# Optimization experiments

Hardware: AMD Instinct MI355X
Metric: run time of the kernel (lower is better)

Reference implementation:

```python
import jax, jax.numpy as jnp
import numpy as np

EPS = 1e-8

def _normalize(a):
    return a / jnp.clip(jnp.linalg.norm(a, axis=-1, keepdims=True), EPS)

def _cosine(a, b):
    # pairwise cosine similarity: [Na, d] x [Nb, d] -> [Na, Nb]
    return _normalize(a) @ _normalize(b).T

def setup_inputs() -> dict:
    key = jax.random.key(0)
    n, k, q, d = 100, 5, 75, 4096
    x = jax.random.normal(key, (n * (k + q), d), dtype=jnp.float32)
    tao = jnp.full((1,), 10.0, dtype=jnp.float32)
    return {"x": x, "tao": tao, "n": n, "k": k, "q": q}

def reference(x, tao, n, k, q):
    d = x.shape[-1]
    x = x.reshape(n, k + q, d)
    support = x[:, :k]                      # [n, k, d]
    query = x[:, k:].reshape(n * q, d)      # [NQ, d]
    NQ = n * q
    proto = support.mean(axis=1)            # [n, d]

    pre_sim = _cosine(query, proto)         # [NQ, n]
    pre_label = jnp.argmax(pre_sim, axis=1) # [NQ]

    # vectorized per-class masked softmax aggregation (replaces Python loop)
    cls_ids = jnp.arange(n)
    mask = pre_label[None, :] == cls_ids[:, None]            # [n, NQ]
    logits_q = jnp.where(mask, pre_sim.T, -jnp.inf)          # [n, NQ]
    proto_n = _normalize(proto)
    self_sim = jnp.sum(proto_n * proto_n, axis=-1)           # [n], cosine(proto, proto)
    logits = jnp.concatenate([logits_q, self_sim[:, None]], axis=1)  # [n, NQ+1]
    w = jax.nn.softmax(logits, axis=1)                       # [n, NQ+1]
    adapted_proto = w[:, :NQ] @ query + w[:, NQ:] * proto    # [n, d]

    sim = _cosine(query, adapted_proto)                      # [NQ, n]
    return tao.reshape(()) * sim
```

## Files before the change

### kernel.cpp

```cpp
#include <hip/hip_runtime.h>
#include <hip/hip_bf16.h>
#include <math.h>

#define NQUERY 7500
#define NCLS   100
#define DIM    4096
#define KQ     75
#define KSUP   5
#define RPC    80
#define MPAD   7552
#define NPAD   112
#define CAPQ   256
#define RCAP   2048
#define EPSF   1e-8f
#define SELEM  845824
#define SLICE_BYTES 3383296u

typedef __attribute__((ext_vector_type(8))) short bf16x8;
typedef __attribute__((ext_vector_type(4))) short s16x4;
typedef __attribute__((ext_vector_type(4))) float f32x4;

__device__ __forceinline__ int xrow_of_query(int j) {
    return (j / KQ) * RPC + KSUP + (j % KQ);
}
__device__ __forceinline__ short bf16t(float x) {
    union { float f; unsigned u; } v; v.f = x;
    return (short)(v.u >> 16);
}
__device__ __forceinline__ float bf16hi(float x) {
    union { float f; unsigned u; } v; v.f = x;
    v.u &= 0xFFFF0000u; return v.f;
}
__device__ __forceinline__ void gload_lds16(const short* g, short* l) {
    __builtin_amdgcn_global_load_lds(
        (const __attribute__((address_space(1))) unsigned int*)g,
        (__attribute__((address_space(3))) unsigned int*)l, 16, 0, 0);
}

__device__ __forceinline__ size_t tile_off(int nt, int lm, int i) {
    return (((size_t)(nt * 128 + (i >> 5)) * 4 + ((i >> 3) & 3)) * 16 + lm) * 8 + (i & 7);
}

__global__ __launch_bounds__(256) void k_proto(const float* __restrict__ x,
        float* __restrict__ proto, short* __restrict__ Phi, short* __restrict__ Plo,
        float* __restrict__ es) {
    const int c = blockIdx.x, t = threadIdx.x;
    const int nt = c >> 4, lm = c & 15;
    if (c >= NCLS) {
        for (int g = t; g < 512; g += 256) {
            const int kstep = g >> 2, kq = g & 3;
            size_t o = (((size_t)(nt * 128 + kstep) * 4 + kq) * 16 + lm) * 8;
            bf16x8 z = {0,0,0,0,0,0,0,0};
            *(bf16x8*)(Phi + o) = z;
            *(bf16x8*)(Plo + o) = z;
        }
        if (t == 0) es[c] = 0.f;
        return;
    }
    __shared__ float red[4];
    __shared__ float s_inv;
    const float* b0 = x + (size_t)(c * RPC) * DIM;
    float v[16];
    float ssq = 0.f;
#pragma unroll
    for (int p = 0; p < 4; ++p) {
        const int i = p * 1024 + t * 4;
        f32x4 s = {0.f, 0.f, 0.f, 0.f};
#pragma unroll
        for (int r = 0; r < KSUP; ++r)
            s += *(const f32x4*)(b0 + (size_t)r * DIM + i);
        s = s / 5.0f;
        *(f32x4*)&v[p*4] = s;
        *(f32x4*)(proto + (size_t)c*DIM + i) = s;
        ssq += s[0]*s[0] + s[1]*s[1] + s[2]*s[2] + s[3]*s[3];
    }
    for (int o = 32; o; o >>= 1) ssq += __shfl_down(ssq, o);
    if ((t & 63) == 0) red[t >> 6] = ssq;
    __syncthreads();
    if (t == 0) {
        float tot = red[0] + red[1] + red[2] + red[3];
        float inv = 1.f / fmaxf(sqrtf(tot), EPSF);
        s_inv = inv;
        es[c] = expf(tot * inv * inv);
    }
    __syncthreads();
    const float inv = s_inv;
#pragma unroll
    for (int p = 0; p < 4; ++p) {
        const int i = p * 1024 + t * 4;
        s16x4 h, l;
#pragma unroll
        for (int e = 0; e < 4; ++e) {
            float pn = v[p*4+e] * inv;
            float hh = bf16hi(pn);
            h[e] = bf16t(pn);
            l[e] = bf16t(pn - hh);
        }
        const size_t o = tile_off(nt, lm, i);
        *(s16x4*)(Phi + o) = h;
        *(s16x4*)(Plo + o) = l;
    }
}

template<int TNKS>
__global__ __launch_bounds__(256) void k_gemm1(const float* __restrict__ x,
        const short* __restrict__ Phi, const short* __restrict__ Plo,
        float* __restrict__ Spart, float* __restrict__ nq2) {
    constexpr int KST = 128 / TNKS;
    constexpr int NG  = KST / 2;
    __shared__ short bbuf[28 * 512];
    const int bx = blockIdx.x, kz = blockIdx.y;
    const int w = threadIdx.x >> 6, lane = threadIdx.x & 63;
    const int lm = lane & 15, kq = lane >> 4;
    const int mt = bx * 4 + w;
    const int j = mt * 16 + lm;
    const int jc = j < NQUERY ? j : NQUERY - 1;
    const float* pa = x + (size_t)xrow_of_query(jc) * DIM + kq * 8;
    const int ks0 = kz * KST;

    f32x4 acc[7];
#pragma unroll
    for (int nt = 0; nt < 7; ++nt) acc[nt] = (f32x4){0.f,0.f,0.f,0.f};
    float ssq = 0.f;

    for (int g = 0; g < NG; ++g) {
        const int gk = ks0 + g * 2;
#pragma unroll
        for (int p = 0; p < 7; ++p) {
            const int cid = w * 7 + p;
            const int s = cid / 14, r = cid % 14, nt = r >> 1, hl = r & 1;
            const short* gsrc = (hl ? Plo : Phi) + ((size_t)(nt * 128 + gk + s) << 9);
            gload_lds16(gsrc + lane * 8, &bbuf[(cid << 9) + lane * 8]);
        }
        __syncthreads();
#pragma unroll
        for (int s = 0; s < 2; ++s) {
            const float* pas = pa + (gk + s) * 32;
            f32x4 f0 = *(const f32x4*)(pas);
            f32x4 f1 = *(const f32x4*)(pas + 4);
            float fv[8] = {f0[0],f0[1],f0[2],f0[3],f1[0],f1[1],f1[2],f1[3]};
            bf16x8 ah, al;
#pragma unroll
            for (int e = 0; e < 8; ++e) {
                float xx = fv[e];
                ssq += xx * xx;
                float hh = bf16hi(xx);
                ah[e] = bf16t(xx);
                al[e] = bf16t(xx - hh);
            }
#pragma unroll
            for (int nt = 0; nt < 7; ++nt) {
                const bf16x8 bh = *(const bf16x8*)(&bbuf[((s*14 + nt*2 + 0) << 9) + lane * 8]);
                const bf16x8 bl = *(const bf16x8*)(&bbuf[((s*14 + nt*2 + 1) << 9) + lane * 8]);
                acc[nt] = __builtin_amdgcn_mfma_f32_16x16x32_bf16(ah, bh, acc[nt], 0, 0, 0);
                acc[nt] = __builtin_amdgcn_mfma_f32_16x16x32_bf16(ah, bl, acc[nt], 0, 0, 0);
                acc[nt] = __builtin_amdgcn_mfma_f32_16x16x32_bf16(al, bh, acc[nt], 0, 0, 0);
            }
        }
        __syncthreads();
    }
    float s2 = ssq;
    s2 += __shfl_xor(s2, 16);
    s2 += __shfl_xor(s2, 32);
    if (kq == 0 && j < NQUERY) atomicAdd(&nq2[j], s2);

    float* sp = Spart + (size_t)kz * SELEM + (size_t)(mt * 16) * NPAD;
#pragma unroll
    for (int nt = 0; nt < 7; ++nt)
#pragma unroll
        for (int r = 0; r < 4; ++r)
            sp[(size_t)(kq * 4 + r) * NPAD + nt * 16 + lm] = acc[nt][r];
}

__global__ __launch_bounds__(256) void k_reduce1(const float* __restrict__ Spart,
        float* __restrict__ Sred, int nks) {
    const int idx = blockIdx.x * 256 + threadIdx.x;
    const size_t e = (size_t)idx * 4;
    f32x4 s = {0.f, 0.f, 0.f, 0.f};
    for (int kz = 0; kz < nks; ++kz)
        s += *(const f32x4*)(Spart + (size_t)kz * SELEM + e);
    *(f32x4*)(Sred + e) = s;
}

__global__ __launch_bounds__(256) void k_argmax(const float* __restrict__ S,
        const float* __restrict__ nq2, int* __restrict__ label, float* __restrict__ coef,
        float* __restrict__ invq, int* __restrict__ rcnt, int* __restrict__ rlist) {
    const int j = blockIdx.x * 256 + threadIdx.x;
    if (j >= NQUERY) return;
    const float* row = S + (size_t)j * NPAD;
    float m1 = -1e30f, m2 = -1e30f;
    int i1 = 0, i2 = 0;
    for (int c = 0; c < NCLS; ++c) {
        float v = row[c];
        if (v > m1) { m2 = m1; i2 = i1; m1 = v; i1 = c; }
        else if (v > m2) { m2 = v; i2 = c; }
    }
    const float inv = 1.f / fmaxf(sqrtf(nq2[j]), EPSF);
    invq[j] = inv;
    label[j] = i1;
    coef[j] = expf(m1 * inv);
    if ((m1 - m2) * inv < 1e-4f) {
        int p = atomicAdd(rcnt, 1);
        if (p < RCAP) rlist[p] = j | (i1 << 13) | (i2 << 20);
    }
}

__global__ __launch_bounds__(64) void k_refine(const float* __restrict__ x,
        const float* __restrict__ S, const float* __restrict__ invq,
        int* __restrict__ label, float* __restrict__ coef,
        const int* __restrict__ rcnt, const int* __restrict__ rlist) {
    const int cnt = min(*rcnt, RCAP);
    const int lane = threadIdx.x;
    for (int e = blockIdx.x; e < cnt; e += gridDim.x) {
        const int pk = rlist[e];
        const int j = pk & 8191, c1 = (pk >> 13) & 127, c2 = (pk >> 20) & 127;
        const float* xq = x + (size_t)xrow_of_query(j) * DIM;
        const int cc[2] = {c1, c2};
        double cosv[2];
#pragma unroll
        for (int s = 0; s < 2; ++s) {
            const float* xb = x + (size_t)(cc[s] * RPC) * DIM;
            double dt = 0.0, pp = 0.0, q2 = 0.0;
            for (int i = lane; i < DIM; i += 64) {
                double p = (double)xb[i] + (double)xb[i + DIM] + (double)xb[i + 2*DIM]
                         + (double)xb[i + 3*DIM] + (double)xb[i + 4*DIM];
                double qv = (double)xq[i];
                dt += p * qv; pp += p * p; q2 += qv * qv;
            }
            for (int o = 32; o; o >>= 1) {
                dt += __shfl_down(dt, o);
                pp += __shfl_down(pp, o);
                q2 += __shfl_down(q2, o);
            }
            cosv[s] = dt / (sqrt(pp) * sqrt(q2));
        }
        if (lane == 0) {
            int win = (cosv[1] > cosv[0] || (cosv[1] == cosv[0] && c2 < c1)) ? c2 : c1;
            if (win != c1) {
                label[j] = win;
                coef[j] = expf(S[(size_t)j * NPAD + win] * invq[j]);
            }
        }
    }
}

__global__ __launch_bounds__(256) void k_lists(const int* __restrict__ label,
        int* __restrict__ cls_cnt, int* __restrict__ cls_list) {
    const int j = blockIdx.x * 256 + threadIdx.x;
    if (j >= NQUERY) return;
    const int c = label[j];
    const int p = atomicAdd(&cls_cnt[c], 1);
    if (p < CAPQ) cls_list[c * CAPQ + p] = j;
}

__global__ __launch_bounds__(128) void k_adapt(const float* __restrict__ x,
        const float* __restrict__ coef, const int* __restrict__ cls_cnt,
        const int* __restrict__ cls_list, float* __restrict__ APpart) {
    const int cx = blockIdx.x, c = blockIdx.y, sl = blockIdx.z;
    const int i0 = cx * 512 + threadIdx.x * 4;
    const int n = min(cls_cnt[c], CAPQ);
    f32x4 acc = {0.f, 0.f, 0.f, 0.f};
    for (int e = sl; e < n; e += 4) {
        const int j = cls_list[c * CAPQ + e];
        const float cf = coef[j];
        const f32x4 v = *(const f32x4*)(x + (size_t)xrow_of_query(j) * DIM + i0);
        acc += v * cf;
    }
    *(f32x4*)(APpart + (size_t)sl * NCLS * DIM + (size_t)c * DIM + i0) = acc;
}

__global__ __launch_bounds__(256) void k_apnorm(const float* __restrict__ APpart,
        const float* __restrict__ proto, const float* __restrict__ es,
        short* __restrict__ APhi) {
    const int c = blockIdx.x, t = threadIdx.x;
    const int nt = c >> 4, lm = c & 15;
    if (c >= NCLS) {
        for (int g = t; g < 512; g += 256) {
            const int kstep = g >> 2, kq = g & 3;
            size_t o = (((size_t)(nt * 128 + kstep) * 4 + kq) * 16 + lm) * 8;
            bf16x8 z = {0,0,0,0,0,0,0,0};
            *(bf16x8*)(APhi + o) = z;
        }
        return;
    }
    __shared__ float red[4];
    __shared__ float s_inv;
    const float e0 = es[c];
    float v[16];
    float ssq = 0.f;
#pragma unroll
    for (int p = 0; p < 4; ++p) {
        const int i = p * 1024 + t * 4;
        f32x4 s = {0.f, 0.f, 0.f, 0.f};
#pragma unroll
        for (int sl = 0; sl < 4; ++sl)
            s += *(const f32x4*)(APpart + (size_t)sl * NCLS * DIM + (size_t)c * DIM + i);
        f32x4 pr = *(const f32x4*)(proto + (size_t)c*DIM + i);
        s += pr * e0;
        *(f32x4*)&v[p*4] = s;
        ssq += s[0]*s[0] + s[1]*s[1] + s[2]*s[2] + s[3]*s[3];
    }
    for (int o = 32; o; o >>= 1) ssq += __shfl_down(ssq, o);
    if ((t & 63) == 0) red[t >> 6] = ssq;
    __syncthreads();
    if (t == 0) {
        float tot = red[0] + red[1] + red[2] + red[3];
        s_inv = 1.f / fmaxf(sqrtf(tot), EPSF);
    }
    __syncthreads();
    const float inv = s_inv;
#pragma unroll
    for (int p = 0; p < 4; ++p) {
        const int i = p * 1024 + t * 4;
        s16x4 h;
#pragma unroll
        for (int e = 0; e < 4; ++e) h[e] = bf16t(v[p*4+e] * inv);
        *(s16x4*)(APhi + tile_off(nt, lm, i)) = h;
    }
}

template<int TNKS>
__global__ __launch_bounds__(256) void k_gemm2(const float* __restrict__ x,
        const short* __restrict__ APhi, float* __restrict__ Opart) {
    constexpr int KST = 128 / TNKS;
    constexpr int NG  = KST / 2;
    __shared__ short bbuf[14 * 512];
    const int bx = blockIdx.x, kz = blockIdx.y;
    const int w = threadIdx.x >> 6, lane = threadIdx.x & 63;
    const int lm = lane & 15, kq = lane >> 4;
    const int mt = bx * 4 + w;
    const int j = mt * 16 + lm;
    const int jc = j < NQUERY ? j : NQUERY - 1;
    const float* pa = x + (size_t)xrow_of_query(jc) * DIM + kq * 8;
    const int ks0 = kz * KST;

    f32x4 acc[7];
#pragma unroll
    for (int nt = 0; nt < 7; ++nt) acc[nt] = (f32x4){0.f,0.f,0.f,0.f};

    for (int g = 0; g < NG; ++g) {
        const int gk = ks0 + g * 2;
#pragma unroll
        for (int p = 0; p < 4; ++p) {
            const int cid = w * 4 + p;
            if (cid < 14) {
                const int s = cid / 7, nt = cid % 7;
                const short* gsrc = APhi + ((size_t)(nt * 128 + gk + s) << 9);
                gload_lds16(gsrc + lane * 8, &bbuf[(cid << 9) + lane * 8]);
            }
        }
        __syncthreads();
#pragma unroll
        for (int s = 0; s < 2; ++s) {
            const float* pas = pa + (gk + s) * 32;
            f32x4 f0 = *(const f32x4*)(pas);
            f32x4 f1 = *(const f32x4*)(pas + 4);
            float fv[8] = {f0[0],f0[1],f0[2],f0[3],f1[0],f1[1],f1[2],f1[3]};
            bf16x8 ah;
#pragma unroll
            for (int e = 0; e < 8; ++e) ah[e] = bf16t(fv[e]);
#pragma unroll
            for (int nt = 0; nt < 7; ++nt) {
                const bf16x8 bh = *(const bf16x8*)(&bbuf[((s*7 + nt) << 9) + lane * 8]);
                acc[nt] = __builtin_amdgcn_mfma_f32_16x16x32_bf16(ah, bh, acc[nt], 0, 0, 0);
            }
        }
        __syncthreads();
    }
    float* op = Opart + (size_t)kz * SELEM + (size_t)(mt * 16) * NPAD;
#pragma unroll
    for (int nt = 0; nt < 7; ++nt)
#pragma unroll
        for (int r = 0; r < 4; ++r)
            op[(size_t)(kq * 4 + r) * NPAD + nt * 16 + lm] = acc[nt][r];
}

__global__ __launch_bounds__(256) void k_reduce2(const float* __restrict__ Opart,
        const float* __restrict__ invq, const float* __restrict__ tao,
        float* __restrict__ out, int nks) {
    const int idx = blockIdx.x * 256 + threadIdx.x;
    if (idx >= NQUERY * 25) return;
    const int j = idx / 25, c4 = (idx % 25) * 4;
    const size_t e = (size_t)j * NPAD + c4;
    f32x4 s = {0.f, 0.f, 0.f, 0.f};
    for (int kz = 0; kz < nks; ++kz)
        s += *(const f32x4*)(Opart + (size_t)kz * SELEM + e);
    const float sc = tao[0] * invq[j];
    *(f32x4*)(out + (size_t)j * NCLS + c4) = s * sc;
}

#define OFF_RCNT   0u
#define OFF_CCNT   256u
#define OFF_NQ2    1792u
#define ZERO_BYTES 32768u
#define OFF_ES     32768u
#define OFF_INVQ   33280u
#define OFF_LABEL  63488u
#define OFF_COEF   93696u
#define OFF_RLIST  123904u
#define OFF_CLIST  132096u
#define OFF_PROTO  234496u
#define OFF_PHI    1872896u
#define OFF_PLO    2790400u
#define OFF_APHI   3707904u
#define OFF_SRED   4625408u
#define OFF_APPART 8008704u
#define OFF_PART   14562304u

extern "C" void kernel_launch(void* const* d_in, const int* in_sizes, int n_in,
                              void* d_out, int out_size, void* d_ws, size_t ws_size,
                              hipStream_t stream) {
    const float* x   = (const float*)d_in[0];
    const float* tao = (const float*)d_in[1];
    char* ws = (char*)d_ws;

    int*   rcnt    = (int*)  (ws + OFF_RCNT);
    int*   ccnt    = (int*)  (ws + OFF_CCNT);
    float* nq2     = (float*)(ws + OFF_NQ2);
    float* es      = (float*)(ws + OFF_ES);
    float* invq    = (float*)(ws + OFF_INVQ);
    int*   label   = (int*)  (ws + OFF_LABEL);
    float* coef    = (float*)(ws + OFF_COEF);
    int*   rlist   = (int*)  (ws + OFF_RLIST);
    int*   clist   = (int*)  (ws + OFF_CLIST);
    float* proto   = (float*)(ws + OFF_PROTO);
    short* Phi     = (short*)(ws + OFF_PHI);
    short* Plo     = (short*)(ws + OFF_PLO);
    short* APhi    = (short*)(ws + OFF_APHI);
    float* Sred    = (float*)(ws + OFF_SRED);
    float* APpart  = (float*)(ws + OFF_APPART);
    float* Part    = (float*)(ws + OFF_PART);

    int nks = 1;
    if (ws_size > (size_t)OFF_PART + SLICE_BYTES) {
        size_t avail = (ws_size - OFF_PART) / SLICE_BYTES;
        nks = avail >= 16 ? 16 : (int)avail;
        while (nks & (nks - 1)) nks &= nks - 1;
    }

    hipMemsetAsync(ws, 0, ZERO_BYTES, stream);

    k_proto <<<NPAD, 256, 0, stream>>>(x, proto, Phi, Plo, es);
    switch (nks) {
        case 16: k_gemm1<16><<<dim3(118, 16), 256, 0, stream>>>(x, Phi, Plo, Part, nq2); break;
        case 8:  k_gemm1<8> <<<dim3(118, 8),  256, 0, stream>>>(x, Phi, Plo, Part, nq2); break;
        case 4:  k_gemm1<4> <<<dim3(118, 4),  256, 0, stream>>>(x, Phi, Plo, Part, nq2); break;
        case 2:  k_gemm1<2> <<<dim3(118, 2),  256, 0, stream>>>(x, Phi, Plo, Part, nq2); break;
        default: k_gemm1<1> <<<dim3(118, 1),  256, 0, stream>>>(x, Phi, Plo, Part, nq2); break;
    }
    k_reduce1<<<826, 256, 0, stream>>>(Part, Sred, nks);
    k_argmax <<<30, 256, 0, stream>>>(Sred, nq2, label, coef, invq, rcnt, rlist);
    k_refine <<<512, 64, 0, stream>>>(x, Sred, invq, label, coef, rcnt, rlist);
    k_lists  <<<30, 256, 0, stream>>>(label, ccnt, clist);
    k_adapt  <<<dim3(8, NCLS, 4), 128, 0, stream>>>(x, coef, ccnt, clist, APpart);
    k_apnorm <<<NPAD, 256, 0, stream>>>(APpart, proto, es, APhi);
    switch (nks) {
        case 16: k_gemm2<16><<<dim3(118, 16), 256, 0, stream>>>(x, APhi, Part); break;
        case 8:  k_gemm2<8> <<<dim3(118, 8),  256, 0, stream>>>(x, APhi, Part); break;
        case 4:  k_gemm2<4> <<<dim3(118, 4),  256, 0, stream>>>(x, APhi, Part); break;
        case 2:  k_gemm2<2> <<<dim3(118, 2),  256, 0, stream>>>(x, APhi, Part); break;
        default: k_gemm2<1> <<<dim3(118, 1),  256, 0, stream>>>(x, APhi, Part); break;
    }
    k_reduce2<<<733, 256, 0, stream>>>(Part, invq, tao, (float*)d_out, nks);
}
```

Measured before the change: 365.1 us.

## Drop split-bf16 first GEMM, unify double-buffered GEMM, fold class lists into argmax

The first similarity GEMM moves from a three-MFMA hi/lo bf16 split to a single bf16 MFMA, so the Plo buffer and its staging go away. Both GEMMs now share one templated kernel that double-buffers the B tile in LDS and prefetches the next A fragment. The per-class list build moves into k_argmax, and k_refine patches the lists for relabelled near-tie queries, which removes the separate k_lists launch. The near-tie threshold is widened to offset the lower argmax precision, at the risk of mislabelling queries or adding more refine work.

```diff
diff --git a/kernel.cpp b/kernel.cpp
--- a/kernel.cpp
+++ b/kernel.cpp
@@ -27,10 +27,6 @@
     union { float f; unsigned u; } v; v.f = x;
     return (short)(v.u >> 16);
 }
-__device__ __forceinline__ float bf16hi(float x) {
-    union { float f; unsigned u; } v; v.f = x;
-    v.u &= 0xFFFF0000u; return v.f;
-}
 __device__ __forceinline__ void gload_lds16(const short* g, short* l) {
     __builtin_amdgcn_global_load_lds(
         (const __attribute__((address_space(1))) unsigned int*)g,
@@ -41,9 +37,20 @@
     return (((size_t)(nt * 128 + (i >> 5)) * 4 + ((i >> 3) & 3)) * 16 + lm) * 8 + (i & 7);
 }
 
+__device__ __forceinline__ void stageB(const short* __restrict__ Bt, int kstep,
+        short* buf, int w, int lane) {
+#pragma unroll
+    for (int p = 0; p < 2; ++p) {
+        const int cid = w * 2 + p;
+        if (cid < 7) {
+            const short* gsrc = Bt + ((size_t)(cid * 128 + kstep) << 9);
+            gload_lds16(gsrc + lane * 8, buf + (cid << 9));
+        }
+    }
+}
+
 __global__ __launch_bounds__(256) void k_proto(const float* __restrict__ x,
-        float* __restrict__ proto, short* __restrict__ Phi, short* __restrict__ Plo,
-        float* __restrict__ es) {
+        float* __restrict__ proto, short* __restrict__ Phi, float* __restrict__ es) {
     const int c = blockIdx.x, t = threadIdx.x;
     const int nt = c >> 4, lm = c & 15;
     if (c >= NCLS) {
@@ -52,7 +59,6 @@
             size_t o = (((size_t)(nt * 128 + kstep) * 4 + kq) * 16 + lm) * 8;
             bf16x8 z = {0,0,0,0,0,0,0,0};
             *(bf16x8*)(Phi + o) = z;
-            *(bf16x8*)(Plo + o) = z;
         }
         if (t == 0) es[c] = 0.f;
         return;
@@ -88,27 +94,18 @@
 #pragma unroll
     for (int p = 0; p < 4; ++p) {
         const int i = p * 1024 + t * 4;
-        s16x4 h, l;
-#pragma unroll
-        for (int e = 0; e < 4; ++e) {
-            float pn = v[p*4+e] * inv;
-            float hh = bf16hi(pn);
-            h[e] = bf16t(pn);
-            l[e] = bf16t(pn - hh);
-        }
-        const size_t o = tile_off(nt, lm, i);
-        *(s16x4*)(Phi + o) = h;
-        *(s16x4*)(Plo + o) = l;
-    }
-}
-
-template<int TNKS>
-__global__ __launch_bounds__(256) void k_gemm1(const float* __restrict__ x,
-        const short* __restrict__ Phi, const short* __restrict__ Plo,
-        float* __restrict__ Spart, float* __restrict__ nq2) {
+        s16x4 h;
+#pragma unroll
+        for (int e = 0; e < 4; ++e) h[e] = bf16t(v[p*4+e] * inv);
+        *(s16x4*)(Phi + tile_off(nt, lm, i)) = h;
+    }
+}
+
+template<int TNKS, bool SSQ>
+__global__ __launch_bounds__(256) void k_gemm(const float* __restrict__ x,
+        const short* __restrict__ Bt, float* __restrict__ Part, float* __restrict__ nq2) {
     constexpr int KST = 128 / TNKS;
-    constexpr int NG  = KST / 2;
-    __shared__ short bbuf[28 * 512];
+    __shared__ short bbuf[2][7 * 512];
     const int bx = blockIdx.x, kz = blockIdx.y;
     const int w = threadIdx.x >> 6, lane = threadIdx.x & 63;
     const int lm = lane & 15, kq = lane >> 4;
@@ -123,48 +120,43 @@
     for (int nt = 0; nt < 7; ++nt) acc[nt] = (f32x4){0.f,0.f,0.f,0.f};
     float ssq = 0.f;
 
-    for (int g = 0; g < NG; ++g) {
-        const int gk = ks0 + g * 2;
-#pragma unroll
-        for (int p = 0; p < 7; ++p) {
-            const int cid = w * 7 + p;
-            const int s = cid / 14, r = cid % 14, nt = r >> 1, hl = r & 1;
-            const short* gsrc = (hl ? Plo : Phi) + ((size_t)(nt * 128 + gk + s) << 9);
-            gload_lds16(gsrc + lane * 8, &bbuf[(cid << 9) + lane * 8]);
+    stageB(Bt, ks0, bbuf[0], w, lane);
+    f32x4 a0 = *(const f32x4*)(pa + ks0 * 32);
+    f32x4 a1 = *(const f32x4*)(pa + ks0 * 32 + 4);
+    __syncthreads();
+
+#pragma unroll
+    for (int s = 0; s < KST; ++s) {
+        const int cur = s & 1;
+        f32x4 n0 = a0, n1 = a1;
+        if (s + 1 < KST) {
+            stageB(Bt, ks0 + s + 1, bbuf[cur ^ 1], w, lane);
+            n0 = *(const f32x4*)(pa + (ks0 + s + 1) * 32);
+            n1 = *(const f32x4*)(pa + (ks0 + s + 1) * 32 + 4);
+        }
+        float fv[8] = {a0[0],a0[1],a0[2],a0[3],a1[0],a1[1],a1[2],a1[3]};
+        bf16x8 ah;
+#pragma unroll
+        for (int e = 0; e < 8; ++e) {
+            if (SSQ) ssq += fv[e] * fv[e];
+            ah[e] = bf16t(fv[e]);
+        }
+#pragma unroll
+        for (int nt = 0; nt < 7; ++nt) {
+            const bf16x8 bh = *(const bf16x8*)(&bbuf[cur][(nt << 9) + lane * 8]);
+            acc[nt] = __builtin_amdgcn_mfma_f32_16x16x32_bf16(ah, bh, acc[nt], 0, 0, 0);
         }
         __syncthreads();
-#pragma unroll
-        for (int s = 0; s < 2; ++s) {
-            const float* pas = pa + (gk + s) * 32;
-            f32x4 f0 = *(const f32x4*)(pas);
-            f32x4 f1 = *(const f32x4*)(pas + 4);
-            float fv[8] = {f0[0],f0[1],f0[2],f0[3],f1[0],f1[1],f1[2],f1[3]};
-            bf16x8 ah, al;
-#pragma unroll
-            for (int e = 0; e < 8; ++e) {
-                float xx = fv[e];
-                ssq += xx * xx;
-                float hh = bf16hi(xx);
-                ah[e] = bf16t(xx);
-                al[e] = bf16t(xx - hh);
-            }
-#pragma unroll
-            for (int nt = 0; nt < 7; ++nt) {
-                const bf16x8 bh = *(const bf16x8*)(&bbuf[((s*14 + nt*2 + 0) << 9) + lane * 8]);
-                const bf16x8 bl = *(const bf16x8*)(&bbuf[((s*14 + nt*2 + 1) << 9) + lane * 8]);
-                acc[nt] = __builtin_amdgcn_mfma_f32_16x16x32_bf16(ah, bh, acc[nt], 0, 0, 0);
-                acc[nt] = __builtin_amdgcn_mfma_f32_16x16x32_bf16(ah, bl, acc[nt], 0, 0, 0);
-                acc[nt] = __builtin_amdgcn_mfma_f32_16x16x32_bf16(al, bh, acc[nt], 0, 0, 0);
-            }
-        }
-        __syncthreads();
-    }
-    float s2 = ssq;
-    s2 += __shfl_xor(s2, 16);
-    s2 += __shfl_xor(s2, 32);
-    if (kq == 0 && j < NQUERY) atomicAdd(&nq2[j], s2);
-
-    float* sp = Spart + (size_t)kz * SELEM + (size_t)(mt * 16) * NPAD;
+        a0 = n0; a1 = n1;
+    }
+
+    if (SSQ) {
+        float s2 = ssq;
+        s2 += __shfl_xor(s2, 16);
+        s2 += __shfl_xor(s2, 32);
+        if (kq == 0 && j < NQUERY) atomicAdd(&nq2[j], s2);
+    }
+    float* sp = Part + (size_t)kz * SELEM + (size_t)(mt * 16) * NPAD;
 #pragma unroll
     for (int nt = 0; nt < 7; ++nt)
 #pragma unroll
@@ -183,8 +175,9 @@
 }
 
 __global__ __launch_bounds__(256) void k_argmax(const float* __restrict__ S,
-        const float* __restrict__ nq2, int* __restrict__ label, float* __restrict__ coef,
-        float* __restrict__ invq, int* __restrict__ rcnt, int* __restrict__ rlist) {
+        const float* __restrict__ nq2, float* __restrict__ coef, float* __restrict__ invq,
+        int* __restrict__ pos, int* __restrict__ ccnt, int* __restrict__ cls_list,
+        int* __restrict__ rcnt, int* __restrict__ rlist) {
     const int j = blockIdx.x * 256 + threadIdx.x;
     if (j >= NQUERY) return;
     const float* row = S + (size_t)j * NPAD;
@@ -197,17 +190,20 @@
     }
     const float inv = 1.f / fmaxf(sqrtf(nq2[j]), EPSF);
     invq[j] = inv;
-    label[j] = i1;
     coef[j] = expf(m1 * inv);
-    if ((m1 - m2) * inv < 1e-4f) {
-        int p = atomicAdd(rcnt, 1);
-        if (p < RCAP) rlist[p] = j | (i1 << 13) | (i2 << 20);
+    const int p = atomicAdd(&ccnt[i1], 1);
+    if (p < CAPQ) { cls_list[i1 * CAPQ + p] = j; pos[j] = p; }
+    else pos[j] = -1;
+    if ((m1 - m2) * inv < 5e-4f) {
+        int rp = atomicAdd(rcnt, 1);
+        if (rp < RCAP) rlist[rp] = j | (i1 << 13) | (i2 << 20);
     }
 }
 
 __global__ __launch_bounds__(64) void k_refine(const float* __restrict__ x,
         const float* __restrict__ S, const float* __restrict__ invq,
-        int* __restrict__ label, float* __restrict__ coef,
+        float* __restrict__ coef, const int* __restrict__ pos,
+        int* __restrict__ ccnt, int* __restrict__ cls_list,
         const int* __restrict__ rcnt, const int* __restrict__ rlist) {
     const int cnt = min(*rcnt, RCAP);
     const int lane = threadIdx.x;
@@ -237,20 +233,14 @@
         if (lane == 0) {
             int win = (cosv[1] > cosv[0] || (cosv[1] == cosv[0] && c2 < c1)) ? c2 : c1;
             if (win != c1) {
-                label[j] = win;
                 coef[j] = expf(S[(size_t)j * NPAD + win] * invq[j]);
+                const int pj = pos[j];
+                if (pj >= 0) cls_list[c1 * CAPQ + pj] = -1;
+                const int np = atomicAdd(&ccnt[c2], 1);
+                if (np < CAPQ) cls_list[c2 * CAPQ + np] = j;
             }
         }
     }
-}
-
-__global__ __launch_bounds__(256) void k_lists(const int* __restrict__ label,
-        int* __restrict__ cls_cnt, int* __restrict__ cls_list) {
-    const int j = blockIdx.x * 256 + threadIdx.x;
-    if (j >= NQUERY) return;
-    const int c = label[j];
-    const int p = atomicAdd(&cls_cnt[c], 1);
-    if (p < CAPQ) cls_list[c * CAPQ + p] = j;
 }
 
 __global__ __launch_bounds__(128) void k_adapt(const float* __restrict__ x,
@@ -262,9 +252,11 @@
     f32x4 acc = {0.f, 0.f, 0.f, 0.f};
     for (int e = sl; e < n; e += 4) {
         const int j = cls_list[c * CAPQ + e];
-        const float cf = coef[j];
-        const f32x4 v = *(const f32x4*)(x + (size_t)xrow_of_query(j) * DIM + i0);
-        acc += v * cf;
+        if (j >= 0) {
+            const float cf = coef[j];
+            const f32x4 v = *(const f32x4*)(x + (size_t)xrow_of_query(j) * DIM + i0);
+            acc += v * cf;
+        }
     }
     *(f32x4*)(APpart + (size_t)sl * NCLS * DIM + (size_t)c * DIM + i0) = acc;
 }
@@ -317,62 +309,6 @@
         for (int e = 0; e < 4; ++e) h[e] = bf16t(v[p*4+e] * inv);
         *(s16x4*)(APhi + tile_off(nt, lm, i)) = h;
     }
-}
-
-template<int TNKS>
-__global__ __launch_bounds__(256) void k_gemm2(const float* __restrict__ x,
-        const short* __restrict__ APhi, float* __restrict__ Opart) {
-    constexpr int KST = 128 / TNKS;
-    constexpr int NG  = KST / 2;
-    __shared__ short bbuf[14 * 512];
-    const int bx = blockIdx.x, kz = blockIdx.y;
-    const int w = threadIdx.x >> 6, lane = threadIdx.x & 63;
-    const int lm = lane & 15, kq = lane >> 4;
-    const int mt = bx * 4 + w;
-    const int j = mt * 16 + lm;
-    const int jc = j < NQUERY ? j : NQUERY - 1;
-    const float* pa = x + (size_t)xrow_of_query(jc) * DIM + kq * 8;
-    const int ks0 = kz * KST;
-
-    f32x4 acc[7];
-#pragma unroll
-    for (int nt = 0; nt < 7; ++nt) acc[nt] = (f32x4){0.f,0.f,0.f,0.f};
-
-    for (int g = 0; g < NG; ++g) {
-        const int gk = ks0 + g * 2;
-#pragma unroll
-        for (int p = 0; p < 4; ++p) {
-            const int cid = w * 4 + p;
-            if (cid < 14) {
-                const int s = cid / 7, nt = cid % 7;
-                const short* gsrc = APhi + ((size_t)(nt * 128 + gk + s) << 9);
-                gload_lds16(gsrc + lane * 8, &bbuf[(cid << 9) + lane * 8]);
-            }
-        }
-        __syncthreads();
-#pragma unroll
-        for (int s = 0; s < 2; ++s) {
-            const float* pas = pa + (gk + s) * 32;
-            f32x4 f0 = *(const f32x4*)(pas);
-            f32x4 f1 = *(const f32x4*)(pas + 4);
-            float fv[8] = {f0[0],f0[1],f0[2],f0[3],f1[0],f1[1],f1[2],f1[3]};
-            bf16x8 ah;
-#pragma unroll
-            for (int e = 0; e < 8; ++e) ah[e] = bf16t(fv[e]);
-#pragma unroll
-            for (int nt = 0; nt < 7; ++nt) {
-                const bf16x8 bh = *(const bf16x8*)(&bbuf[((s*7 + nt) << 9) + lane * 8]);
-                acc[nt] = __builtin_amdgcn_mfma_f32_16x16x32_bf16(ah, bh, acc[nt], 0, 0, 0);
-            }
-        }
-        __syncthreads();
-    }
-    float* op = Opart + (size_t)kz * SELEM + (size_t)(mt * 16) * NPAD;
-#pragma unroll
-    for (int nt = 0; nt < 7; ++nt)
-#pragma unroll
-        for (int r = 0; r < 4; ++r)
-            op[(size_t)(kq * 4 + r) * NPAD + nt * 16 + lm] = acc[nt][r];
 }
 
 __global__ __launch_bounds__(256) void k_reduce2(const float* __restrict__ Opart,
@@ -395,13 +331,12 @@
 #define ZERO_BYTES 32768u
 #define OFF_ES     32768u
 #define OFF_INVQ   33280u
-#define OFF_LABEL  63488u
+#define OFF_POS    63488u
 #define OFF_COEF   93696u
 #define OFF_RLIST  123904u
 #define OFF_CLIST  132096u
 #define OFF_PROTO  234496u
 #define OFF_PHI    1872896u
-#define OFF_PLO    2790400u
 #define OFF_APHI   3707904u
 #define OFF_SRED   4625408u
 #define OFF_APPART 8008704u
@@ -419,13 +354,12 @@
     float* nq2     = (float*)(ws + OFF_NQ2);
     float* es      = (float*)(ws + OFF_ES);
     float* invq    = (float*)(ws + OFF_INVQ);
-    int*   label   = (int*)  (ws + OFF_LABEL);
+    int*   pos     = (int*)  (ws + OFF_POS);
     float* coef    = (float*)(ws + OFF_COEF);
     int*   rlist   = (int*)  (ws + OFF_RLIST);
     int*   clist   = (int*)  (ws + OFF_CLIST);
     float* proto   = (float*)(ws + OFF_PROTO);
     short* Phi     = (short*)(ws + OFF_PHI);
-    short* Plo     = (short*)(ws + OFF_PLO);
     short* APhi    = (short*)(ws + OFF_APHI);
     float* Sred    = (float*)(ws + OFF_SRED);
     float* APpart  = (float*)(ws + OFF_APPART);
@@ -440,26 +374,25 @@
 
     hipMemsetAsync(ws, 0, ZERO_BYTES, stream);
 
-    k_proto <<<NPAD, 256, 0, stream>>>(x, proto, Phi, Plo, es);
+    k_proto <<<NPAD, 256, 0, stream>>>(x, proto, Phi, es);
     switch (nks) {
-        case 16: k_gemm1<16><<<dim3(118, 16), 256, 0, stream>>>(x, Phi, Plo, Part, nq2); break;
-        case 8:  k_gemm1<8> <<<dim3(118, 8),  256, 0, stream>>>(x, Phi, Plo, Part, nq2); break;
-        case 4:  k_gemm1<4> <<<dim3(118, 4),  256, 0, stream>>>(x, Phi, Plo, Part, nq2); break;
-        case 2:  k_gemm1<2> <<<dim3(118, 2),  256, 0, stream>>>(x, Phi, Plo, Part, nq2); break;
-        default: k_gemm1<1> <<<dim3(118, 1),  256, 0, stream>>>(x, Phi, Plo, Part, nq2); break;
+        case 16: k_gemm<16,true><<<dim3(118, 16), 256, 0, stream>>>(x, Phi, Part, nq2); break;
+        case 8:  k_gemm<8, true><<<dim3(118, 8),  256, 0, stream>>>(x, Phi, Part, nq2); break;
+        case 4:  k_gemm<4, true><<<dim3(118, 4),  256, 0, stream>>>(x, Phi, Part, nq2); break;
+        case 2:  k_gemm<2, true><<<dim3(118, 2),  256, 0, stream>>>(x, Phi, Part, nq2); break;
+        default: k_gemm<1, true><<<dim3(118, 1),  256, 0, stream>>>(x, Phi, Part, nq2); break;
     }
     k_reduce1<<<826, 256, 0, stream>>>(Part, Sred, nks);
-    k_argmax <<<30, 256, 0, stream>>>(Sred, nq2, label, coef, invq, rcnt, rlist);
-    k_refine <<<512, 64, 0, stream>>>(x, Sred, invq, label, coef, rcnt, rlist);
-    k_lists  <<<30, 256, 0, stream>>>(label, ccnt, clist);
+    k_argmax <<<30, 256, 0, stream>>>(Sred, nq2, coef, invq, pos, ccnt, clist, rcnt, rlist);
+    k_refine <<<512, 64, 0, stream>>>(x, Sred, invq, coef, pos, ccnt, clist, rcnt, rlist);
     k_adapt  <<<dim3(8, NCLS, 4), 128, 0, stream>>>(x, coef, ccnt, clist, APpart);
     k_apnorm <<<NPAD, 256, 0, stream>>>(APpart, proto, es, APhi);
     switch (nks) {
-        case 16: k_gemm2<16><<<dim3(118, 16), 256, 0, stream>>>(x, APhi, Part); break;
-        case 8:  k_gemm2<8> <<<dim3(118, 8),  256, 0, stream>>>(x, APhi, Part); break;
-        case 4:  k_gemm2<4> <<<dim3(118, 4),  256, 0, stream>>>(x, APhi, Part); break;
-        case 2:  k_gemm2<2> <<<dim3(118, 2),  256, 0, stream>>>(x, APhi, Part); break;
-        default: k_gemm2<1> <<<dim3(118, 1),  256, 0, stream>>>(x, APhi, Part); break;
+        case 16: k_gemm<16,false><<<dim3(118, 16), 256, 0, stream>>>(x, APhi, Part, nq2); break;
+        case 8:  k_gemm<8, false><<<dim3(118, 8),  256, 0, stream>>>(x, APhi, Part, nq2); break;
+        case 4:  k_gemm<4, false><<<dim3(118, 4),  256, 0, stream>>>(x, APhi, Part, nq2); break;
+        case 2:  k_gemm<2, false><<<dim3(118, 2),  256, 0, stream>>>(x, APhi, Part, nq2); break;
+        default: k_gemm<1, false><<<dim3(118, 1),  256, 0, stream>>>(x, APhi, Part, nq2); break;
     }
     k_reduce2<<<733, 256, 0, stream>>>(Part, invq, tao, (float*)d_out, nks);
 }
```

Result: slower. 403.2 us (+10.4%).
